# Optimization experiments

Hardware: AMD Instinct MI355X
Metric: run time of the kernel (lower is better)

Reference implementation:

```python
import jax, jax.numpy as jnp
import numpy as np

HEADS = 8

def _proj(x, W, b):
    # 1x1 conv == per-pixel linear: x [B,C,H,W], W [O,C], b [O]
    return jnp.einsum('bchw,oc->bohw', x, W) + b[None, :, None, None]

def setup_inputs() -> dict:
    key = jax.random.key(0)
    ks = jax.random.split(key, 9)
    B, C, H, W = 8, 256, 32, 32
    s = C ** -0.5
    return {
        'x':  jax.random.normal(ks[0], (B, C, H, W), jnp.float32),
        'Wq': jax.random.normal(ks[1], (C, C), jnp.float32) * s,
        'bq': jax.random.normal(ks[2], (C,), jnp.float32) * 0.02,
        'Wk': jax.random.normal(ks[3], (C, C), jnp.float32) * s,
        'bk': jax.random.normal(ks[4], (C,), jnp.float32) * 0.02,
        'Wv': jax.random.normal(ks[5], (C, C), jnp.float32) * s,
        'bv': jax.random.normal(ks[6], (C,), jnp.float32) * 0.02,
        'Wm': jax.random.normal(ks[7], (C, C), jnp.float32) * s,
        'bm': jax.random.normal(ks[8], (C,), jnp.float32) * 0.02,
    }

def reference(x, Wq, bq, Wk, bk, Wv, bv, Wm, bm):
    B, C, H, W = x.shape
    h = HEADS
    hd = C // h
    scale = hd ** -0.5

    def to_heads(t):
        # [B,C,H,W] -> [B,h,hd,H,W] -> [B,h,HW,hd]
        t = t.reshape(B, h, hd, H, W)
        return t.transpose(0, 1, 3, 4, 2).reshape(B, h, H * W, hd)

    q = to_heads(_proj(x, Wq, bq))
    k = to_heads(_proj(x, Wk, bk))
    v = to_heads(_proj(x, Wv, bv))

    attn = jax.nn.softmax(jnp.einsum('bhnd,bhmd->bhnm', q, k) * scale, axis=-1)
    out = jnp.einsum('bhnm,bhmd->bhnd', attn, v)          # [B,h,HW,hd]
    # torch: view(B,h,H,W,hd).permute(0,4,1,2,3).view(B,C,H,W) => channel = d*h + head
    out = out.reshape(B, h, H, W, hd).transpose(0, 4, 1, 2, 3).reshape(B, C, H, W)
    return _proj(out, Wm, bm)
```

## Files before the change

kernel.cpp:

```cpp
#include <hip/hip_runtime.h>
#include <cstdint>
#include <cstddef>


#define NB 8
#define NC 256
#define NP 1024
#define NHD 8
#define HD 32

typedef short bf16x8 __attribute__((ext_vector_type(8)));
typedef float f32x4 __attribute__((ext_vector_type(4)));

#define SCLLOG 0.25505654356918f

__device__ __forceinline__ unsigned cvt_pk_bf16(float a, float b) {
  unsigned r;
  asm("v_cvt_pk_bf16_f32 %0, %1, %2" : "=v"(r) : "v"(a), "v"(b));
  return r;
}
__device__ __forceinline__ unsigned short f2b1(float a) {
  return (unsigned short)cvt_pk_bf16(a, a);
}

__global__ __launch_bounds__(256) void prep_kernel(
    const float* __restrict__ Wq, const float* __restrict__ Wk,
    const float* __restrict__ Wv, const float* __restrict__ Wm,
    const float* __restrict__ x, unsigned short* __restrict__ Wb,
    unsigned short* __restrict__ xt) {
  __shared__ float sx[64][65];
  int bx = blockIdx.x, tid = threadIdx.x;
  if (bx < 128) {
    int idx = (bx * 256 + tid) * 8;
    const float* src; int off;
    if (idx < 65536)       { src = Wq; off = idx; }
    else if (idx < 131072) { src = Wk; off = idx - 65536; }
    else if (idx < 196608) { src = Wv; off = idx - 131072; }
    else                   { src = Wm; off = idx - 196608; }
    float4 lo = *(const float4*)(src + off);
    float4 hi = *(const float4*)(src + off + 4);
    union { unsigned u[4]; bf16x8 v; } o;
    o.u[0] = cvt_pk_bf16(lo.x, lo.y); o.u[1] = cvt_pk_bf16(lo.z, lo.w);
    o.u[2] = cvt_pk_bf16(hi.x, hi.y); o.u[3] = cvt_pk_bf16(hi.z, hi.w);
    *(bf16x8*)(Wb + idx) = o.v;
  } else {
    int bi = bx - 128;
    int b = bi >> 6, rest = bi & 63;
    int ct = (rest & 3) * 64, pt = (rest >> 2) * 64;
    const float* xb = x + ((size_t)(b * NC + ct)) * NP + pt;
    int pr = (tid & 15) * 4, cr = tid >> 4;
#pragma unroll
    for (int i = 0; i < 4; i++) {
      float4 v = *(const float4*)(xb + (size_t)(cr + i * 16) * NP + pr);
      sx[cr + i*16][pr]   = v.x; sx[cr + i*16][pr+1] = v.y;
      sx[cr + i*16][pr+2] = v.z; sx[cr + i*16][pr+3] = v.w;
    }
    __syncthreads();
    int pl = tid >> 3, cc = (tid & 7) * 8;
#pragma unroll
    for (int j = 0; j < 2; j++) {
      int p = pl + j * 32;
      union { unsigned u[4]; bf16x8 v; } o;
#pragma unroll
      for (int u = 0; u < 4; u++)
        o.u[u] = cvt_pk_bf16(sx[cc + 2*u][p], sx[cc + 2*u + 1][p]);
      *(bf16x8*)(xt + ((size_t)b * NP + pt + p) * NC + ct + cc) = o.v;
    }
  }
}

__global__ __launch_bounds__(256) void qkv_kernel(
    const unsigned short* __restrict__ Wb,
    const float* __restrict__ bq, const float* __restrict__ bk,
    const float* __restrict__ bv,
    const unsigned short* __restrict__ xt,
    unsigned short* __restrict__ qt, unsigned short* __restrict__ kt,
    unsigned short* __restrict__ vt) {
  int proj = blockIdx.z, b = blockIdx.y, bx = blockIdx.x;
  int ot = (bx & 3) * 64, pt = (bx >> 2) * 64;
  int tid = threadIdx.x, wave = tid >> 6, lane = tid & 63;
  int l15 = lane & 15, quad = lane >> 4;
  int oW = ot + (wave & 1) * 32, pW = pt + (wave >> 1) * 32;
  const unsigned short* W = Wb + (size_t)proj * 65536;
  const float* bias = (proj == 0) ? bq : (proj == 1) ? bk : bv;
  const unsigned short* A0 = W + (size_t)(oW + l15) * NC + quad * 8;
  const unsigned short* B0 = xt + ((size_t)b * NP + pW + l15) * NC + quad * 8;
  f32x4 acc[2][2];
#pragma unroll
  for (int i = 0; i < 2; i++)
#pragma unroll
    for (int j = 0; j < 2; j++) acc[i][j] = (f32x4){0.f, 0.f, 0.f, 0.f};
#pragma unroll
  for (int c0 = 0; c0 < NC; c0 += 32) {
    bf16x8 a0 = *(const bf16x8*)(A0 + c0);
    bf16x8 a1 = *(const bf16x8*)(A0 + 16 * NC + c0);
    bf16x8 b0 = *(const bf16x8*)(B0 + c0);
    bf16x8 b1 = *(const bf16x8*)(B0 + 16 * NC + c0);
    acc[0][0] = __builtin_amdgcn_mfma_f32_16x16x32_bf16(a0, b0, acc[0][0], 0, 0, 0);
    acc[0][1] = __builtin_amdgcn_mfma_f32_16x16x32_bf16(a0, b1, acc[0][1], 0, 0, 0);
    acc[1][0] = __builtin_amdgcn_mfma_f32_16x16x32_bf16(a1, b0, acc[1][0], 0, 0, 0);
    acc[1][1] = __builtin_amdgcn_mfma_f32_16x16x32_bf16(a1, b1, acc[1][1], 0, 0, 0);
  }
  unsigned short* qk = (proj == 0) ? qt : kt;
#pragma unroll
  for (int rh = 0; rh < 2; rh++) {
    int od0 = oW + rh * 16 + quad * 4;
    float b0 = bias[od0], b1 = bias[od0+1], b2 = bias[od0+2], b3 = bias[od0+3];
#pragma unroll
    for (int ch = 0; ch < 2; ch++) {
      float v0 = acc[rh][ch][0] + b0, v1 = acc[rh][ch][1] + b1;
      float v2 = acc[rh][ch][2] + b2, v3 = acc[rh][ch][3] + b3;
      if (proj < 2) {
        int p = pW + ch * 16 + l15;
        int h2 = od0 >> 5, d0 = od0 & 31;
        uint2 pk;
        pk.x = cvt_pk_bf16(v0, v1);
        pk.y = cvt_pk_bf16(v2, v3);
        size_t idx = ((size_t)(b * NHD + h2) * NP + p) * HD + d0;
        *(uint2*)(qk + idx) = pk;
      } else {
        int p2 = pW + 2 * l15 + ch;
        size_t base = ((size_t)b * NC + od0) * NP + p2;
        vt[base]          = f2b1(v0);
        vt[base +     NP] = f2b1(v1);
        vt[base + 2 * NP] = f2b1(v2);
        vt[base + 3 * NP] = f2b1(v3);
      }
    }
  }
}

__global__ __launch_bounds__(512) void attn_kernel(
    const unsigned short* __restrict__ qt, const unsigned short* __restrict__ kt,
    const unsigned short* __restrict__ vt, unsigned short* __restrict__ at) {
  int tid = threadIdx.x, wave = tid >> 6, lane = tid & 63;
  int l15 = lane & 15, quad = lane >> 4;
  int half = wave >> 2, wsub = wave & 3;
  int bh = blockIdx.y, b = bh >> 3, h = bh & 7;
  int n0 = blockIdx.x * 128 + wsub * 32;
  __shared__ __align__(16) unsigned short P[8][1280];
  __shared__ float Comb[4][64][25];
  unsigned short* Pw = &P[wave][0];

  bf16x8 qfa = *(const bf16x8*)(qt + ((size_t)bh * NP + n0 + l15) * HD + quad * 8);
  bf16x8 qfb = *(const bf16x8*)(qt + ((size_t)bh * NP + n0 + 16 + l15) * HD + quad * 8);
  const unsigned short* kp = kt + (size_t)bh * NP * HD + (size_t)l15 * HD + quad * 8;
  const unsigned short* vp = vt + ((size_t)(b * NC + h * HD) + l15) * NP + quad * 8;

  union { unsigned u[4]; bf16x8 v; } ones;
  ones.u[0] = ones.u[1] = ones.u[2] = ones.u[3] = 0x3F803F80u;

  f32x4 oa0 = (f32x4){0.f,0.f,0.f,0.f}, oa1 = (f32x4){0.f,0.f,0.f,0.f};
  f32x4 ob0 = (f32x4){0.f,0.f,0.f,0.f}, ob1 = (f32x4){0.f,0.f,0.f,0.f};
  f32x4 la  = (f32x4){0.f,0.f,0.f,0.f}, lb  = (f32x4){0.f,0.f,0.f,0.f};
  const f32x4 z = (f32x4){0.f,0.f,0.f,0.f};

  int mbase = half * 512;
  bf16x8 kf0 = *(const bf16x8*)(kp + mbase * HD);
  bf16x8 kf1 = *(const bf16x8*)(kp + (mbase + 16) * HD);
  bf16x8 vf0 = *(const bf16x8*)(vp + mbase);
  bf16x8 vf1 = *(const bf16x8*)(vp + 16 * NP + mbase);

  for (int m0 = mbase; m0 < mbase + 512; m0 += 32) {
    f32x4 s0a = __builtin_amdgcn_mfma_f32_16x16x32_bf16(qfa, kf0, z, 0, 0, 0);
    f32x4 s1a = __builtin_amdgcn_mfma_f32_16x16x32_bf16(qfa, kf1, z, 0, 0, 0);
    f32x4 s0b = __builtin_amdgcn_mfma_f32_16x16x32_bf16(qfb, kf0, z, 0, 0, 0);
    f32x4 s1b = __builtin_amdgcn_mfma_f32_16x16x32_bf16(qfb, kf1, z, 0, 0, 0);
    bf16x8 nk0 = *(const bf16x8*)(kp + (m0 + 32) * HD);
    bf16x8 nk1 = *(const bf16x8*)(kp + (m0 + 48) * HD);
    bf16x8 nv0 = *(const bf16x8*)(vp + m0 + 32);
    bf16x8 nv1 = *(const bf16x8*)(vp + 16 * NP + m0 + 32);
#pragma unroll
    for (int r = 0; r < 4; r++) {
      float pa0 = __builtin_amdgcn_exp2f(fmaf(s0a[r], SCLLOG, -16.0f));
      float pa1 = __builtin_amdgcn_exp2f(fmaf(s1a[r], SCLLOG, -16.0f));
      float pb0 = __builtin_amdgcn_exp2f(fmaf(s0b[r], SCLLOG, -16.0f));
      float pb1 = __builtin_amdgcn_exp2f(fmaf(s1b[r], SCLLOG, -16.0f));
      *(unsigned*)(Pw + (quad * 4 + r) * 40 + 2 * l15)       = cvt_pk_bf16(pa0, pa1);
      *(unsigned*)(Pw + 640 + (quad * 4 + r) * 40 + 2 * l15) = cvt_pk_bf16(pb0, pb1);
    }
    bf16x8 pfa = *(const bf16x8*)(Pw + l15 * 40 + quad * 8);
    bf16x8 pfb = *(const bf16x8*)(Pw + 640 + l15 * 40 + quad * 8);
    oa0 = __builtin_amdgcn_mfma_f32_16x16x32_bf16(pfa, vf0, oa0, 0, 0, 0);
    oa1 = __builtin_amdgcn_mfma_f32_16x16x32_bf16(pfa, vf1, oa1, 0, 0, 0);
    ob0 = __builtin_amdgcn_mfma_f32_16x16x32_bf16(pfb, vf0, ob0, 0, 0, 0);
    ob1 = __builtin_amdgcn_mfma_f32_16x16x32_bf16(pfb, vf1, ob1, 0, 0, 0);
    la  = __builtin_amdgcn_mfma_f32_16x16x32_bf16(pfa, ones.v, la, 0, 0, 0);
    lb  = __builtin_amdgcn_mfma_f32_16x16x32_bf16(pfb, ones.v, lb, 0, 0, 0);
    kf0 = nk0; kf1 = nk1; vf0 = nv0; vf1 = nv1;
  }

  if (half == 1) {
    float* C = &Comb[wsub][lane][0];
#pragma unroll
    for (int r = 0; r < 4; r++) {
      C[r]      = oa0[r];  C[4 + r]  = oa1[r];
      C[8 + r]  = ob0[r];  C[12 + r] = ob1[r];
      C[16 + r] = la[r];   C[20 + r] = lb[r];
    }
  }
  __syncthreads();
  if (half == 0) {
    const float* C = &Comb[wsub][lane][0];
#pragma unroll
    for (int r = 0; r < 4; r++) {
      oa0[r] += C[r];      oa1[r] += C[4 + r];
      ob0[r] += C[8 + r];  ob1[r] += C[12 + r];
      la[r]  += C[16 + r]; lb[r]  += C[20 + r];
    }
    unsigned short* ab = at + (size_t)b * NP * NC;
#pragma unroll
    for (int r = 0; r < 4; r++) {
      float inva = 1.0f / la[r], invb = 1.0f / lb[r];
      int na = n0 + quad * 4 + r, nb = n0 + 16 + quad * 4 + r;
      ab[(size_t)na * NC + (l15 * 8 + h)]        = f2b1(oa0[r] * inva);
      ab[(size_t)na * NC + ((16 + l15) * 8 + h)] = f2b1(oa1[r] * inva);
      ab[(size_t)nb * NC + (l15 * 8 + h)]        = f2b1(ob0[r] * invb);
      ab[(size_t)nb * NC + ((16 + l15) * 8 + h)] = f2b1(ob1[r] * invb);
    }
  }
}

__global__ __launch_bounds__(256) void mproj_kernel(
    const unsigned short* __restrict__ Wmb, const float* __restrict__ bm,
    const unsigned short* __restrict__ at, float* __restrict__ out) {
  int b = blockIdx.y, bx = blockIdx.x;
  int ot = (bx & 3) * 64, pt = (bx >> 2) * 64;
  int tid = threadIdx.x, wave = tid >> 6, lane = tid & 63;
  int l15 = lane & 15, quad = lane >> 4;
  int oW = ot + (wave & 1) * 32, pW = pt + (wave >> 1) * 32;
  const unsigned short* A0 = Wmb + (size_t)(oW + l15) * NC + quad * 8;
  const unsigned short* B0 = at + ((size_t)b * NP + pW + l15) * NC + quad * 8;
  f32x4 acc[2][2];
#pragma unroll
  for (int i = 0; i < 2; i++)
#pragma unroll
    for (int j = 0; j < 2; j++) acc[i][j] = (f32x4){0.f, 0.f, 0.f, 0.f};
#pragma unroll
  for (int c0 = 0; c0 < NC; c0 += 32) {
    bf16x8 a0 = *(const bf16x8*)(A0 + c0);
    bf16x8 a1 = *(const bf16x8*)(A0 + 16 * NC + c0);
    bf16x8 b0 = *(const bf16x8*)(B0 + c0);
    bf16x8 b1 = *(const bf16x8*)(B0 + 16 * NC + c0);
    acc[0][0] = __builtin_amdgcn_mfma_f32_16x16x32_bf16(a0, b0, acc[0][0], 0, 0, 0);
    acc[0][1] = __builtin_amdgcn_mfma_f32_16x16x32_bf16(a0, b1, acc[0][1], 0, 0, 0);
    acc[1][0] = __builtin_amdgcn_mfma_f32_16x16x32_bf16(a1, b0, acc[1][0], 0, 0, 0);
    acc[1][1] = __builtin_amdgcn_mfma_f32_16x16x32_bf16(a1, b1, acc[1][1], 0, 0, 0);
  }
#pragma unroll
  for (int rh = 0; rh < 2; rh++) {
    int od0 = oW + rh * 16 + quad * 4;
    float b0 = bm[od0], b1 = bm[od0+1], b2 = bm[od0+2], b3 = bm[od0+3];
#pragma unroll
    for (int ch = 0; ch < 2; ch++) {
      int p = pW + ch * 16 + l15;
      size_t base = ((size_t)b * NC + od0) * NP + p;
      out[base]          = acc[rh][ch][0] + b0;
      out[base +     NP] = acc[rh][ch][1] + b1;
      out[base + 2 * NP] = acc[rh][ch][2] + b2;
      out[base + 3 * NP] = acc[rh][ch][3] + b3;
    }
  }
}

extern "C" void kernel_launch(void* const* d_in, const int* in_sizes, int n_in,
                              void* d_out, int out_size, void* d_ws, size_t ws_size,
                              hipStream_t stream) {
  (void)in_sizes; (void)n_in; (void)out_size; (void)ws_size;
  const float* x  = (const float*)d_in[0];
  const float* Wq = (const float*)d_in[1];
  const float* bq = (const float*)d_in[2];
  const float* Wk = (const float*)d_in[3];
  const float* bk = (const float*)d_in[4];
  const float* Wv = (const float*)d_in[5];
  const float* bv = (const float*)d_in[6];
  const float* Wm = (const float*)d_in[7];
  const float* bm = (const float*)d_in[8];
  float* out = (float*)d_out;
  char* ws = (char*)d_ws;

  unsigned short* xt = (unsigned short*)(ws);
  unsigned short* Wb = (unsigned short*)(ws + (4u << 20));
  unsigned short* qt = (unsigned short*)(ws + (4u << 20) + (512u << 10));
  unsigned short* kt = (unsigned short*)(ws + (8u << 20) + (512u << 10));
  unsigned short* vt = (unsigned short*)(ws + (12u << 20) + (512u << 10));
  unsigned short* at = (unsigned short*)(ws + (16u << 20) + (512u << 10));

  prep_kernel<<<640, 256, 0, stream>>>(Wq, Wk, Wv, Wm, x, Wb, xt);
  qkv_kernel<<<dim3(64, 8, 3), 256, 0, stream>>>(Wb, bq, bk, bv, xt, qt, kt, vt);
  attn_kernel<<<dim3(8, 64), 512, 0, stream>>>(qt, kt, vt, at);
  mproj_kernel<<<dim3(64, 8), 256, 0, stream>>>(Wb + 3 * 65536, bm, at, out);
}
```

Baseline: 139.0 us.

## Keep attention probabilities in registers using transposed 32x32 MFMA and lane swaps

The attention kernel now computes S transposed (K·Q) with 32x32x16 bf16 MFMAs. Probabilities are repacked in registers using v_permlane32_swap, so they go straight into the PV MFMA instead of round-tripping through LDS. The softmax scale is folded into Q during the QKV projection, and the V store layout is changed to match the new operand layout. Row sums now come from VALU adds instead of an extra ones-MFMA. Blocks shrink to 256 threads with a two-way split over keys, and the fixed -16 exponent offset is dropped, which carries some overflow risk for larger scores.

```diff
diff --git a/kernel.cpp b/kernel.cpp
--- a/kernel.cpp
+++ b/kernel.cpp
@@ -11,8 +11,11 @@
 
 typedef short bf16x8 __attribute__((ext_vector_type(8)));
 typedef float f32x4 __attribute__((ext_vector_type(4)));
+typedef float f32x16 __attribute__((ext_vector_type(16)));
 
 #define SCLLOG 0.25505654356918f
+
+#define F32X16_ZERO (f32x16){0.f,0.f,0.f,0.f,0.f,0.f,0.f,0.f,0.f,0.f,0.f,0.f,0.f,0.f,0.f,0.f}
 
 __device__ __forceinline__ unsigned cvt_pk_bf16(float a, float b) {
   unsigned r;
@@ -83,6 +86,7 @@
   int oW = ot + (wave & 1) * 32, pW = pt + (wave >> 1) * 32;
   const unsigned short* W = Wb + (size_t)proj * 65536;
   const float* bias = (proj == 0) ? bq : (proj == 1) ? bk : bv;
+  float sc = (proj == 0) ? SCLLOG : 1.0f;
   const unsigned short* A0 = W + (size_t)(oW + l15) * NC + quad * 8;
   const unsigned short* B0 = xt + ((size_t)b * NP + pW + l15) * NC + quad * 8;
   f32x4 acc[2][2];
@@ -110,17 +114,16 @@
     for (int ch = 0; ch < 2; ch++) {
       float v0 = acc[rh][ch][0] + b0, v1 = acc[rh][ch][1] + b1;
       float v2 = acc[rh][ch][2] + b2, v3 = acc[rh][ch][3] + b3;
+      int p = pW + ch * 16 + l15;
       if (proj < 2) {
-        int p = pW + ch * 16 + l15;
         int h2 = od0 >> 5, d0 = od0 & 31;
         uint2 pk;
-        pk.x = cvt_pk_bf16(v0, v1);
-        pk.y = cvt_pk_bf16(v2, v3);
+        pk.x = cvt_pk_bf16(v0 * sc, v1 * sc);
+        pk.y = cvt_pk_bf16(v2 * sc, v3 * sc);
         size_t idx = ((size_t)(b * NHD + h2) * NP + p) * HD + d0;
         *(uint2*)(qk + idx) = pk;
       } else {
-        int p2 = pW + 2 * l15 + ch;
-        size_t base = ((size_t)b * NC + od0) * NP + p2;
+        size_t base = ((size_t)b * NC + od0) * NP + p;
         vt[base]          = f2b1(v0);
         vt[base +     NP] = f2b1(v1);
         vt[base + 2 * NP] = f2b1(v2);
@@ -130,93 +133,84 @@
   }
 }
 
-__global__ __launch_bounds__(512) void attn_kernel(
+__global__ __launch_bounds__(256, 4) void attn_kernel(
     const unsigned short* __restrict__ qt, const unsigned short* __restrict__ kt,
     const unsigned short* __restrict__ vt, unsigned short* __restrict__ at) {
   int tid = threadIdx.x, wave = tid >> 6, lane = tid & 63;
-  int l15 = lane & 15, quad = lane >> 4;
-  int half = wave >> 2, wsub = wave & 3;
+  int l31 = lane & 31, hi = lane >> 5;
+  int half = wave >> 1, wsub = wave & 1;
   int bh = blockIdx.y, b = bh >> 3, h = bh & 7;
-  int n0 = blockIdx.x * 128 + wsub * 32;
-  __shared__ __align__(16) unsigned short P[8][1280];
-  __shared__ float Comb[4][64][25];
-  unsigned short* Pw = &P[wave][0];
-
-  bf16x8 qfa = *(const bf16x8*)(qt + ((size_t)bh * NP + n0 + l15) * HD + quad * 8);
-  bf16x8 qfb = *(const bf16x8*)(qt + ((size_t)bh * NP + n0 + 16 + l15) * HD + quad * 8);
-  const unsigned short* kp = kt + (size_t)bh * NP * HD + (size_t)l15 * HD + quad * 8;
-  const unsigned short* vp = vt + ((size_t)(b * NC + h * HD) + l15) * NP + quad * 8;
-
-  union { unsigned u[4]; bf16x8 v; } ones;
-  ones.u[0] = ones.u[1] = ones.u[2] = ones.u[3] = 0x3F803F80u;
-
-  f32x4 oa0 = (f32x4){0.f,0.f,0.f,0.f}, oa1 = (f32x4){0.f,0.f,0.f,0.f};
-  f32x4 ob0 = (f32x4){0.f,0.f,0.f,0.f}, ob1 = (f32x4){0.f,0.f,0.f,0.f};
-  f32x4 la  = (f32x4){0.f,0.f,0.f,0.f}, lb  = (f32x4){0.f,0.f,0.f,0.f};
-  const f32x4 z = (f32x4){0.f,0.f,0.f,0.f};
+  int n0 = blockIdx.x * 64 + wsub * 32;
+
+  __shared__ float Comb[2][64][17];
+  __shared__ float Linv[2][32];
+
+  const unsigned short* qp = qt + ((size_t)bh * NP + n0 + l31) * HD + hi * 8;
+  bf16x8 qf0 = *(const bf16x8*)(qp);
+  bf16x8 qf1 = *(const bf16x8*)(qp + 16);
+
+  const unsigned short* kp = kt + ((size_t)bh * NP + l31) * HD + hi * 8;
+  const unsigned short* vp = vt + ((size_t)(b * NC + h * HD + l31)) * NP + hi * 8;
+
+  f32x16 oacc = F32X16_ZERO;
+  f32x4 la = (f32x4){0.f, 0.f, 0.f, 0.f};
 
   int mbase = half * 512;
-  bf16x8 kf0 = *(const bf16x8*)(kp + mbase * HD);
-  bf16x8 kf1 = *(const bf16x8*)(kp + (mbase + 16) * HD);
+  bf16x8 kf0 = *(const bf16x8*)(kp + (size_t)mbase * HD);
+  bf16x8 kf1 = *(const bf16x8*)(kp + (size_t)mbase * HD + 16);
   bf16x8 vf0 = *(const bf16x8*)(vp + mbase);
-  bf16x8 vf1 = *(const bf16x8*)(vp + 16 * NP + mbase);
+  bf16x8 vf1 = *(const bf16x8*)(vp + mbase + 16);
 
   for (int m0 = mbase; m0 < mbase + 512; m0 += 32) {
-    f32x4 s0a = __builtin_amdgcn_mfma_f32_16x16x32_bf16(qfa, kf0, z, 0, 0, 0);
-    f32x4 s1a = __builtin_amdgcn_mfma_f32_16x16x32_bf16(qfa, kf1, z, 0, 0, 0);
-    f32x4 s0b = __builtin_amdgcn_mfma_f32_16x16x32_bf16(qfb, kf0, z, 0, 0, 0);
-    f32x4 s1b = __builtin_amdgcn_mfma_f32_16x16x32_bf16(qfb, kf1, z, 0, 0, 0);
-    bf16x8 nk0 = *(const bf16x8*)(kp + (m0 + 32) * HD);
-    bf16x8 nk1 = *(const bf16x8*)(kp + (m0 + 48) * HD);
+    f32x16 s = __builtin_amdgcn_mfma_f32_32x32x16_bf16(kf0, qf0, F32X16_ZERO, 0, 0, 0);
+    s = __builtin_amdgcn_mfma_f32_32x32x16_bf16(kf1, qf1, s, 0, 0, 0);
+    bf16x8 nk0 = *(const bf16x8*)(kp + (size_t)(m0 + 32) * HD);
+    bf16x8 nk1 = *(const bf16x8*)(kp + (size_t)(m0 + 32) * HD + 16);
     bf16x8 nv0 = *(const bf16x8*)(vp + m0 + 32);
-    bf16x8 nv1 = *(const bf16x8*)(vp + 16 * NP + m0 + 32);
-#pragma unroll
-    for (int r = 0; r < 4; r++) {
-      float pa0 = __builtin_amdgcn_exp2f(fmaf(s0a[r], SCLLOG, -16.0f));
-      float pa1 = __builtin_amdgcn_exp2f(fmaf(s1a[r], SCLLOG, -16.0f));
-      float pb0 = __builtin_amdgcn_exp2f(fmaf(s0b[r], SCLLOG, -16.0f));
-      float pb1 = __builtin_amdgcn_exp2f(fmaf(s1b[r], SCLLOG, -16.0f));
-      *(unsigned*)(Pw + (quad * 4 + r) * 40 + 2 * l15)       = cvt_pk_bf16(pa0, pa1);
-      *(unsigned*)(Pw + 640 + (quad * 4 + r) * 40 + 2 * l15) = cvt_pk_bf16(pb0, pb1);
-    }
-    bf16x8 pfa = *(const bf16x8*)(Pw + l15 * 40 + quad * 8);
-    bf16x8 pfb = *(const bf16x8*)(Pw + 640 + l15 * 40 + quad * 8);
-    oa0 = __builtin_amdgcn_mfma_f32_16x16x32_bf16(pfa, vf0, oa0, 0, 0, 0);
-    oa1 = __builtin_amdgcn_mfma_f32_16x16x32_bf16(pfa, vf1, oa1, 0, 0, 0);
-    ob0 = __builtin_amdgcn_mfma_f32_16x16x32_bf16(pfb, vf0, ob0, 0, 0, 0);
-    ob1 = __builtin_amdgcn_mfma_f32_16x16x32_bf16(pfb, vf1, ob1, 0, 0, 0);
-    la  = __builtin_amdgcn_mfma_f32_16x16x32_bf16(pfa, ones.v, la, 0, 0, 0);
-    lb  = __builtin_amdgcn_mfma_f32_16x16x32_bf16(pfb, ones.v, lb, 0, 0, 0);
+    bf16x8 nv1 = *(const bf16x8*)(vp + m0 + 48);
+    float p[16];
+#pragma unroll
+    for (int r = 0; r < 16; r++) p[r] = __builtin_amdgcn_exp2f(s[r]);
+#pragma unroll
+    for (int r = 0; r < 16; r++) la[r & 3] += p[r];
+    unsigned w0 = cvt_pk_bf16(p[0],  p[1]),  w1 = cvt_pk_bf16(p[2],  p[3]);
+    unsigned w2 = cvt_pk_bf16(p[4],  p[5]),  w3 = cvt_pk_bf16(p[6],  p[7]);
+    unsigned w4 = cvt_pk_bf16(p[8],  p[9]),  w5 = cvt_pk_bf16(p[10], p[11]);
+    unsigned w6 = cvt_pk_bf16(p[12], p[13]), w7 = cvt_pk_bf16(p[14], p[15]);
+    asm("v_permlane32_swap_b32 %0, %1" : "+v"(w0), "+v"(w2));
+    asm("v_permlane32_swap_b32 %0, %1" : "+v"(w1), "+v"(w3));
+    asm("v_permlane32_swap_b32 %0, %1" : "+v"(w4), "+v"(w6));
+    asm("v_permlane32_swap_b32 %0, %1" : "+v"(w5), "+v"(w7));
+    union { unsigned u[4]; bf16x8 v; } pa0, pa1;
+    pa0.u[0] = w0; pa0.u[1] = w1; pa0.u[2] = w2; pa0.u[3] = w3;
+    pa1.u[0] = w4; pa1.u[1] = w5; pa1.u[2] = w6; pa1.u[3] = w7;
+    oacc = __builtin_amdgcn_mfma_f32_32x32x16_bf16(pa0.v, vf0, oacc, 0, 0, 0);
+    oacc = __builtin_amdgcn_mfma_f32_32x32x16_bf16(pa1.v, vf1, oacc, 0, 0, 0);
     kf0 = nk0; kf1 = nk1; vf0 = nv0; vf1 = nv1;
   }
 
+  float lsum = (la[0] + la[1]) + (la[2] + la[3]);
+  lsum += __shfl_xor(lsum, 32, 64);
+
   if (half == 1) {
-    float* C = &Comb[wsub][lane][0];
-#pragma unroll
-    for (int r = 0; r < 4; r++) {
-      C[r]      = oa0[r];  C[4 + r]  = oa1[r];
-      C[8 + r]  = ob0[r];  C[12 + r] = ob1[r];
-      C[16 + r] = la[r];   C[20 + r] = lb[r];
-    }
+    float* Cb = &Comb[wsub][lane][0];
+#pragma unroll
+    for (int r = 0; r < 16; r++) Cb[r] = oacc[r];
+    Cb[16] = lsum;
   }
   __syncthreads();
   if (half == 0) {
-    const float* C = &Comb[wsub][lane][0];
-#pragma unroll
-    for (int r = 0; r < 4; r++) {
-      oa0[r] += C[r];      oa1[r] += C[4 + r];
-      ob0[r] += C[8 + r];  ob1[r] += C[12 + r];
-      la[r]  += C[16 + r]; lb[r]  += C[20 + r];
-    }
-    unsigned short* ab = at + (size_t)b * NP * NC;
-#pragma unroll
-    for (int r = 0; r < 4; r++) {
-      float inva = 1.0f / la[r], invb = 1.0f / lb[r];
-      int na = n0 + quad * 4 + r, nb = n0 + 16 + quad * 4 + r;
-      ab[(size_t)na * NC + (l15 * 8 + h)]        = f2b1(oa0[r] * inva);
-      ab[(size_t)na * NC + ((16 + l15) * 8 + h)] = f2b1(oa1[r] * inva);
-      ab[(size_t)nb * NC + (l15 * 8 + h)]        = f2b1(ob0[r] * invb);
-      ab[(size_t)nb * NC + ((16 + l15) * 8 + h)] = f2b1(ob1[r] * invb);
+    const float* Cb = &Comb[wsub][lane][0];
+#pragma unroll
+    for (int r = 0; r < 16; r++) oacc[r] += Cb[r];
+    lsum += Cb[16];
+    if (hi == 0) Linv[wsub][l31] = 1.0f / lsum;
+    unsigned short* ab = at + (size_t)b * NP * NC + (size_t)(l31 * 8 + h);
+#pragma unroll
+    for (int r = 0; r < 16; r++) {
+      int crow = (r & 3) + 8 * (r >> 2) + 4 * hi;
+      float iv = Linv[wsub][crow];
+      ab[(size_t)(n0 + crow) * NC] = f2b1(oacc[r] * iv);
     }
   }
 }
@@ -288,6 +282,6 @@
 
   prep_kernel<<<640, 256, 0, stream>>>(Wq, Wk, Wv, Wm, x, Wb, xt);
   qkv_kernel<<<dim3(64, 8, 3), 256, 0, stream>>>(Wb, bq, bk, bv, xt, qt, kt, vt);
-  attn_kernel<<<dim3(8, 64), 512, 0, stream>>>(qt, kt, vt, at);
+  attn_kernel<<<dim3(16, 64), 256, 0, stream>>>(qt, kt, vt, at);
   mproj_kernel<<<dim3(64, 8), 256, 0, stream>>>(Wb + 3 * 65536, bm, at, out);
 }
```

Result: faster. 135.9 us (-2.3%).
